# Performance work log

Measured on AMD Instinct MI355X. Metric: run time of the kernel, lower is better.

## Reference

```python
import jax, jax.numpy as jnp
import numpy as np

E = 800_000      # number of edges
D = 256          # d_model_edge
N = 50_000       # number of atoms/nodes


def setup_inputs() -> dict:
    key = jax.random.key(0)
    k1, k2, k3, k4, k5 = jax.random.split(key, 5)
    forces = jax.random.normal(k1, (E, D), dtype=jnp.float32)
    V_st = jax.random.normal(k2, (E, 3), dtype=jnp.float32)
    # MLP([D, D, 1]): Linear(D,D) + act + Linear(D,1). Scaled init for stability.
    W1 = jax.random.normal(k3, (D, D), dtype=jnp.float32) * (1.0 / np.sqrt(D))
    b1 = jnp.zeros((D,), dtype=jnp.float32)
    W2 = jax.random.normal(k4, (D, 1), dtype=jnp.float32) * (1.0 / np.sqrt(D))
    b2 = jnp.zeros((1,), dtype=jnp.float32)
    idx_t = jax.random.randint(k5, (E,), 0, N, dtype=jnp.int64 if jax.config.jax_enable_x64 else jnp.int32)
    return {
        "forces": forces,
        "V_st": V_st,
        "W1": W1,
        "b1": b1,
        "W2": W2,
        "b2": b2,
        "idx_t": idx_t,
        "n_atoms": N,
    }


def reference(forces, V_st, W1, b1, W2, b2, idx_t, n_atoms):
    # out_mlp: Linear(D,D) -> SiLU -> Linear(D,1)
    h = jax.nn.silu(forces @ W1 + b1)          # [E, D]
    s = h @ W2 + b2                            # [E, 1] per-edge scalar
    ev = s * V_st                              # [E, 3] scaled direction vectors
    # scatter-sum over target node indices (reduction='sum')
    out = jax.ops.segment_sum(ev, idx_t, num_segments=n_atoms)  # [N, 3]
    return out
```

## Files before the change

kernel.cpp:

```cpp
#include <hip/hip_runtime.h>
#include <hip/hip_bf16.h>

typedef __attribute__((ext_vector_type(8))) short short8;
typedef __attribute__((ext_vector_type(4))) float floatx4;
typedef unsigned short u16;

#define D 256
#define BM 64
#define NT 256
#define NBLK 512

__device__ __forceinline__ short f2bf(float f) {
    return __builtin_bit_cast(short, __float2bfloat16(f));
}

__global__ void prep_kernel(const float* __restrict__ W1, u16* __restrict__ W1F,
                            float* __restrict__ out, int outn) {
    const int b = blockIdx.x;
    if (b < D) {
        const int k = b, n = threadIdx.x;
        const int k0t = k >> 5, g = (k >> 3) & 3, j = k & 7;
        const int nt = n >> 4, l15 = n & 15;
        W1F[(long)((((k0t << 4) + nt) << 6) + (g << 4) + l15) * 8 + j] = (u16)f2bf(W1[k * D + n]);
    } else {
        int i = (b - D) * 256 + threadIdx.x;
        const int stride = (gridDim.x - D) * 256;
        for (; i < outn; i += stride) out[i] = 0.f;
    }
}

struct R8 { floatx4 f0, f1; };

__launch_bounds__(NT, 2)
__global__ void head_kernel(const float* __restrict__ forces,
                            const float* __restrict__ V_st,
                            const u16*   __restrict__ W1F,
                            const float* __restrict__ b1,
                            const float* __restrict__ W2,
                            const float* __restrict__ b2,
                            const int*   __restrict__ idx_t,
                            float* __restrict__ out,
                            int E) {
    __shared__ u16 Albs[32 * 512];
    __shared__ float s_red[4][BM];

    const int tid  = threadIdx.x;
    const int lane = tid & 63;
    const int wq   = tid >> 6;
    const int l15  = lane & 15;
    const int g    = lane >> 4;
    const int ntiles = E / BM;

    short8 bfr[32];
#pragma unroll
    for (int k0t = 0; k0t < 8; ++k0t)
#pragma unroll
        for (int nc = 0; nc < 4; ++nc)
            bfr[k0t * 4 + nc] =
                *(const short8*)(W1F + (long)((k0t * 16 + wq * 4 + nc) * 64 + lane) * 8);

    float b1v[4], w2v[4];
#pragma unroll
    for (int nc = 0; nc < 4; ++nc) {
        int n = wq * 64 + nc * 16 + l15;
        b1v[nc] = b1[n];
        w2v[nc] = W2[n];
    }
    const float b2v = b2[0];

    const int arow = tid >> 2;
    const int agg  = tid & 3;
    const int aslot = ((agg << 4) | (arow & 15)) * 8;
    const int art   = arow >> 4;

    for (long t = blockIdx.x; t < (long)ntiles; t += NBLK) {
        const long row0 = t * BM;

        float vx = 0.f, vy = 0.f, vz = 0.f;
        int nd = -1;
        if (lane < 16) {
            long e = row0 + wq * 16 + lane;
            vx = V_st[e * 3 + 0]; vy = V_st[e * 3 + 1]; vz = V_st[e * 3 + 2];
            nd = idx_t[e];
        }

        const float* abase = forces + (row0 + arow) * (long)D + agg * 8;
        R8 r[8];
#pragma unroll
        for (int k0t = 0; k0t < 8; ++k0t) {
            r[k0t].f0 = *(const floatx4*)(abase + k0t * 32);
            r[k0t].f1 = *(const floatx4*)(abase + k0t * 32 + 4);
        }
#pragma unroll
        for (int k0t = 0; k0t < 8; ++k0t) {
            short8 a;
#pragma unroll
            for (int j = 0; j < 4; ++j) { a[j] = f2bf(r[k0t].f0[j]); a[4 + j] = f2bf(r[k0t].f1[j]); }
            *(short8*)&Albs[(k0t * 4 + art) * 512 + aslot] = a;
        }
        __syncthreads();

        floatx4 acc[4][4];
#pragma unroll
        for (int rt = 0; rt < 4; ++rt)
#pragma unroll
            for (int nc = 0; nc < 4; ++nc)
                acc[rt][nc] = (floatx4){0.f, 0.f, 0.f, 0.f};

#pragma unroll
        for (int k0t = 0; k0t < 8; ++k0t) {
            short8 af[4];
#pragma unroll
            for (int rt = 0; rt < 4; ++rt)
                af[rt] = *(const short8*)&Albs[(k0t * 4 + rt) * 512 + lane * 8];
#pragma unroll
            for (int rt = 0; rt < 4; ++rt)
#pragma unroll
                for (int nc = 0; nc < 4; ++nc)
                    acc[rt][nc] = __builtin_amdgcn_mfma_f32_16x16x32_bf16(
                        af[rt], bfr[k0t * 4 + nc], acc[rt][nc], 0, 0, 0);
        }

        float part[4][4];
#pragma unroll
        for (int rt = 0; rt < 4; ++rt)
#pragma unroll
            for (int rr = 0; rr < 4; ++rr) {
                float sv = 0.f;
#pragma unroll
                for (int nc = 0; nc < 4; ++nc) {
                    float z = acc[rt][nc][rr] + b1v[nc];
                    float h = z / (1.f + __expf(-z));
                    sv += h * w2v[nc];
                }
                part[rt][rr] = sv;
            }

#pragma unroll
        for (int off = 1; off < 16; off <<= 1)
#pragma unroll
            for (int rt = 0; rt < 4; ++rt)
#pragma unroll
                for (int rr = 0; rr < 4; ++rr)
                    part[rt][rr] += __shfl_xor(part[rt][rr], off, 16);

        if (l15 == 0) {
#pragma unroll
            for (int rt = 0; rt < 4; ++rt)
#pragma unroll
                for (int rr = 0; rr < 4; ++rr)
                    s_red[wq][rt * 16 + g * 4 + rr] = part[rt][rr];
        }
        __syncthreads();

        if (nd >= 0) {
            int row = wq * 16 + lane;
            float sv = s_red[0][row] + s_red[1][row] + s_red[2][row] + s_red[3][row] + b2v;
            atomicAdd(&out[(long)nd * 3 + 0], sv * vx);
            atomicAdd(&out[(long)nd * 3 + 1], sv * vy);
            atomicAdd(&out[(long)nd * 3 + 2], sv * vz);
        }
    }
}

extern "C" void kernel_launch(void* const* d_in, const int* in_sizes, int n_in,
                              void* d_out, int out_size, void* d_ws, size_t ws_size,
                              hipStream_t stream) {
    const float* forces = (const float*)d_in[0];
    const float* V_st   = (const float*)d_in[1];
    const float* W1     = (const float*)d_in[2];
    const float* b1     = (const float*)d_in[3];
    const float* W2     = (const float*)d_in[4];
    const float* b2     = (const float*)d_in[5];
    const int*   idx    = (const int*)d_in[6];
    const int E = in_sizes[6];

    u16* W1F = (u16*)d_ws;

    prep_kernel<<<D + 128, 256, 0, stream>>>(W1, W1F, (float*)d_out, out_size);
    head_kernel<<<NBLK, NT, 0, stream>>>(forces, V_st, W1F, b1, W2, b2, idx,
                                         (float*)d_out, E);
}
```

Baseline: 295.6 us.

## Double-buffer A tiles with register prefetch and stream W1 fragments from memory

Halves the row tile to 32 edges and doubles the block count with occupancy 4. The next tile's forces are prefetched into registers while the current tile runs its MFMAs, then written to the other LDS buffer, so one barrier per tile replaces two. W1 fragments are no longer held in registers; they are reloaded from global/L2 on every k-step to free VGPRs for the higher occupancy. The cost is repeated W1 traffic per tile and more atomic and loop overhead from the smaller tiles.

```diff
diff --git a/kernel.cpp b/kernel.cpp
--- a/kernel.cpp
+++ b/kernel.cpp
@@ -6,9 +6,9 @@
 typedef unsigned short u16;
 
 #define D 256
-#define BM 64
+#define BM 32
 #define NT 256
-#define NBLK 512
+#define NBLK 1024
 
 __device__ __forceinline__ short f2bf(float f) {
     return __builtin_bit_cast(short, __float2bfloat16(f));
@@ -29,9 +29,7 @@
     }
 }
 
-struct R8 { floatx4 f0, f1; };
-
-__launch_bounds__(NT, 2)
+__launch_bounds__(NT, 4)
 __global__ void head_kernel(const float* __restrict__ forces,
                             const float* __restrict__ V_st,
                             const u16*   __restrict__ W1F,
@@ -41,8 +39,8 @@
                             const int*   __restrict__ idx_t,
                             float* __restrict__ out,
                             int E) {
-    __shared__ u16 Albs[32 * 512];
-    __shared__ float s_red[4][BM];
+    __shared__ u16 Albs[2][16 * 512];
+    __shared__ float s_red[2][4][BM];
 
     const int tid  = threadIdx.x;
     const int lane = tid & 63;
@@ -50,14 +48,18 @@
     const int l15  = lane & 15;
     const int g    = lane >> 4;
     const int ntiles = E / BM;
-
-    short8 bfr[32];
-#pragma unroll
-    for (int k0t = 0; k0t < 8; ++k0t)
-#pragma unroll
-        for (int nc = 0; nc < 4; ++nc)
-            bfr[k0t * 4 + nc] =
-                *(const short8*)(W1F + (long)((k0t * 16 + wq * 4 + nc) * 64 + lane) * 8);
+    const long b = blockIdx.x;
+    const int niter = (int)(((long)ntiles - b + NBLK - 1) / NBLK);
+
+    const int arow = tid >> 3;
+    const int s8   = tid & 7;
+    int asl[4];
+#pragma unroll
+    for (int j = 0; j < 4; ++j) {
+        int gp = s8 + 8 * j;
+        int f  = (gp >> 2) * 2 + (arow >> 4);
+        asl[j] = f * 512 + (((gp & 3) << 4) | (arow & 15)) * 8;
+    }
 
     float b1v[4], w2v[4];
 #pragma unroll
@@ -68,62 +70,78 @@
     }
     const float b2v = b2[0];
 
-    const int arow = tid >> 2;
-    const int agg  = tid & 3;
-    const int aslot = ((agg << 4) | (arow & 15)) * 8;
-    const int art   = arow >> 4;
-
-    for (long t = blockIdx.x; t < (long)ntiles; t += NBLK) {
-        const long row0 = t * BM;
+    auto LOADA = [&](long tile, floatx4* r0, floatx4* r1) {
+        const float* src = forces + (tile * BM + arow) * (long)D;
+#pragma unroll
+        for (int j = 0; j < 4; ++j) {
+            int gp = s8 + 8 * j;
+            r0[j] = *(const floatx4*)(src + gp * 8);
+            r1[j] = *(const floatx4*)(src + gp * 8 + 4);
+        }
+    };
+    auto CVTW = [&](int buf, const floatx4* r0, const floatx4* r1) {
+#pragma unroll
+        for (int j = 0; j < 4; ++j) {
+            short8 a;
+#pragma unroll
+            for (int q = 0; q < 4; ++q) { a[q] = f2bf(r0[j][q]); a[4 + q] = f2bf(r1[j][q]); }
+            *(short8*)&Albs[buf][asl[j]] = a;
+        }
+    };
+
+    {
+        floatx4 r0[4], r1[4];
+        LOADA(b, r0, r1);
+        CVTW(0, r0, r1);
+    }
+    asm volatile("s_waitcnt lgkmcnt(0)" ::: "memory");
+    __builtin_amdgcn_s_barrier();
+    asm volatile("" ::: "memory");
+    __builtin_amdgcn_sched_barrier(0);
+
+    for (int i = 0; i < niter; ++i) {
+        const long t   = b + (long)i * NBLK;
+        const int  cur = i & 1;
+        const bool more = (i + 1) < niter;
 
         float vx = 0.f, vy = 0.f, vz = 0.f;
         int nd = -1;
-        if (lane < 16) {
-            long e = row0 + wq * 16 + lane;
+        if (tid < BM) {
+            long e = t * BM + tid;
             vx = V_st[e * 3 + 0]; vy = V_st[e * 3 + 1]; vz = V_st[e * 3 + 2];
             nd = idx_t[e];
         }
-
-        const float* abase = forces + (row0 + arow) * (long)D + agg * 8;
-        R8 r[8];
-#pragma unroll
-        for (int k0t = 0; k0t < 8; ++k0t) {
-            r[k0t].f0 = *(const floatx4*)(abase + k0t * 32);
-            r[k0t].f1 = *(const floatx4*)(abase + k0t * 32 + 4);
-        }
-#pragma unroll
-        for (int k0t = 0; k0t < 8; ++k0t) {
-            short8 a;
-#pragma unroll
-            for (int j = 0; j < 4; ++j) { a[j] = f2bf(r[k0t].f0[j]); a[4 + j] = f2bf(r[k0t].f1[j]); }
-            *(short8*)&Albs[(k0t * 4 + art) * 512 + aslot] = a;
-        }
-        __syncthreads();
-
-        floatx4 acc[4][4];
-#pragma unroll
-        for (int rt = 0; rt < 4; ++rt)
+        floatx4 r0[4], r1[4];
+        if (more) LOADA(t + NBLK, r0, r1);
+        __builtin_amdgcn_sched_barrier(0);
+
+        floatx4 acc[2][4];
+#pragma unroll
+        for (int rt = 0; rt < 2; ++rt)
 #pragma unroll
             for (int nc = 0; nc < 4; ++nc)
                 acc[rt][nc] = (floatx4){0.f, 0.f, 0.f, 0.f};
 
 #pragma unroll
         for (int k0t = 0; k0t < 8; ++k0t) {
-            short8 af[4];
-#pragma unroll
-            for (int rt = 0; rt < 4; ++rt)
-                af[rt] = *(const short8*)&Albs[(k0t * 4 + rt) * 512 + lane * 8];
-#pragma unroll
-            for (int rt = 0; rt < 4; ++rt)
+            short8 bf[4], af[2];
+#pragma unroll
+            for (int nc = 0; nc < 4; ++nc)
+                bf[nc] = *(const short8*)(W1F + (long)((k0t * 16 + wq * 4 + nc) * 64 + lane) * 8);
+#pragma unroll
+            for (int rt = 0; rt < 2; ++rt)
+                af[rt] = *(const short8*)&Albs[cur][(k0t * 2 + rt) * 512 + lane * 8];
+#pragma unroll
+            for (int rt = 0; rt < 2; ++rt)
 #pragma unroll
                 for (int nc = 0; nc < 4; ++nc)
                     acc[rt][nc] = __builtin_amdgcn_mfma_f32_16x16x32_bf16(
-                        af[rt], bfr[k0t * 4 + nc], acc[rt][nc], 0, 0, 0);
-        }
-
-        float part[4][4];
-#pragma unroll
-        for (int rt = 0; rt < 4; ++rt)
+                        af[rt], bf[nc], acc[rt][nc], 0, 0, 0);
+        }
+
+        float part[2][4];
+#pragma unroll
+        for (int rt = 0; rt < 2; ++rt)
 #pragma unroll
             for (int rr = 0; rr < 4; ++rr) {
                 float sv = 0.f;
@@ -135,27 +153,31 @@
                 }
                 part[rt][rr] = sv;
             }
-
 #pragma unroll
         for (int off = 1; off < 16; off <<= 1)
 #pragma unroll
-            for (int rt = 0; rt < 4; ++rt)
+            for (int rt = 0; rt < 2; ++rt)
 #pragma unroll
                 for (int rr = 0; rr < 4; ++rr)
                     part[rt][rr] += __shfl_xor(part[rt][rr], off, 16);
-
         if (l15 == 0) {
 #pragma unroll
-            for (int rt = 0; rt < 4; ++rt)
+            for (int rt = 0; rt < 2; ++rt)
 #pragma unroll
                 for (int rr = 0; rr < 4; ++rr)
-                    s_red[wq][rt * 16 + g * 4 + rr] = part[rt][rr];
-        }
-        __syncthreads();
+                    s_red[cur][wq][rt * 16 + g * 4 + rr] = part[rt][rr];
+        }
+
+        if (more) CVTW(cur ^ 1, r0, r1);
+
+        asm volatile("s_waitcnt lgkmcnt(0)" ::: "memory");
+        __builtin_amdgcn_s_barrier();
+        asm volatile("" ::: "memory");
+        __builtin_amdgcn_sched_barrier(0);
 
         if (nd >= 0) {
-            int row = wq * 16 + lane;
-            float sv = s_red[0][row] + s_red[1][row] + s_red[2][row] + s_red[3][row] + b2v;
+            float sv = s_red[cur][0][tid] + s_red[cur][1][tid]
+                     + s_red[cur][2][tid] + s_red[cur][3][tid] + b2v;
             atomicAdd(&out[(long)nd * 3 + 0], sv * vx);
             atomicAdd(&out[(long)nd * 3 + 1], sv * vy);
             atomicAdd(&out[(long)nd * 3 + 2], sv * vz);
```

Result: slower. 758.0 us (+156.5%).
